# Kernel tuning notes

Hardware: AMD Instinct MI355X
Metric: run time of the kernel (lower is better)

Reference implementation:

```python
import jax, jax.numpy as jnp
import numpy as np

B, S, D_MODEL = 8, 2048, 512
G, V = 2, 320          # num_groups, num_vars
CV_DIM = 256 // G      # proj_dim // num_groups = 128
TAU = 2.0


def setup_inputs() -> dict:
    key = jax.random.key(0)
    k1, k2, k3, k4, k5 = jax.random.split(key, 5)
    hidden_states = jax.random.normal(k1, (B, S, D_MODEL), dtype=jnp.float32)
    # Linear(d_model -> G*V); store as (in, out) for direct matmul
    W = jax.random.normal(k2, (D_MODEL, G * V), dtype=jnp.float32) * (1.0 / np.sqrt(D_MODEL))
    b = jax.random.normal(k3, (G * V,), dtype=jnp.float32) * 0.01
    codevectors = jax.random.normal(k4, (1, G * V, CV_DIM), dtype=jnp.float32)
    # pre-sampled Gumbel(0,1) noise, shape (B*S*G, V)
    u = jax.random.uniform(k5, (B * S * G, V), dtype=jnp.float32,
                           minval=1e-10, maxval=1.0)
    gumbels = -jnp.log(-jnp.log(u))
    return {"hidden_states": hidden_states, "W": W, "b": b,
            "codevectors": codevectors, "gumbels": gumbels}


def reference(hidden_states, W, b, codevectors, gumbels):
    Bs, Ss, _ = hidden_states.shape
    N = Bs * Ss
    # weight projection: (B,S,D) @ (D,G*V) -> (B,S,G*V)
    logits = hidden_states @ W + b
    logits = logits.reshape(N * G, V).astype(jnp.float32)

    # gumbel-softmax, hard=True with straight-through
    y_soft = jax.nn.softmax((logits + gumbels) / TAU, axis=-1)  # (N*G, V)
    idx = jnp.argmax(y_soft, axis=-1)
    y_hard = jax.nn.one_hot(idx, V, dtype=y_soft.dtype)
    codevector_probs = y_hard - jax.lax.stop_gradient(y_soft) + y_soft

    # perplexity from the (noise-free) soft distribution
    soft_dist = jax.nn.softmax(logits.reshape(N, G, V), axis=-1)
    marginal = soft_dist.mean(axis=0)                            # (G, V)
    perplexity = jnp.exp(-jnp.sum(marginal * jnp.log(marginal + 1e-7),
                                  axis=-1)).sum()

    # codebook lookup as weighted sum (equivalent to one-hot gather)
    cv = codevectors.reshape(G, V, CV_DIM)
    probs = codevector_probs.reshape(N, G, V)
    out = jnp.einsum('ngv,gvd->ngd', probs, cv)                  # (N, G, d)
    out = out.reshape(Bs, Ss, G * CV_DIM)
    return out, perplexity
```

## Files before the change

kernel.cpp:

```cpp
#include <hip/hip_runtime.h>

#define M_ROWS 16384
#define K_DIM  512
#define N_COLS 640
#define V_CODES 320
#define CV_DIM 128

typedef _Float16 half8 __attribute__((ext_vector_type(8)));
typedef _Float16 half4v __attribute__((ext_vector_type(4)));
typedef float floatx4 __attribute__((ext_vector_type(4)));

__device__ inline void gll16(const void* g, void* l) {
    __builtin_amdgcn_global_load_lds(
        (const __attribute__((address_space(1))) void*)g,
        (__attribute__((address_space(3))) void*)l, 16, 0, 0);
}

#define SBAR()  __builtin_amdgcn_sched_barrier(0)
#define WAITV(N) asm volatile("s_waitcnt vmcnt(" #N ")" ::: "memory")
#define WAITL() asm volatile("s_waitcnt lgkmcnt(0)" ::: "memory")

__global__ __launch_bounds__(256)
void prepW(const float* __restrict__ W, _Float16* __restrict__ Wt,
           float* __restrict__ marginal) {
    __shared__ float tile[32][33];
    const int b = blockIdx.x, t = threadIdx.x;
    if (b == 320) {
        for (int i = t; i < 640; i += 256) marginal[i] = 0.f;
        return;
    }
    const int n0 = (b % 20) * 32, k0 = (b / 20) * 32;
    {
        const int kk = t >> 3, nn4 = (t & 7) << 2;
        const float4 w = *(const float4*)(W + (size_t)(k0 + kk) * 640 + n0 + nn4);
        tile[kk][nn4 + 0] = w.x; tile[kk][nn4 + 1] = w.y;
        tile[kk][nn4 + 2] = w.z; tile[kk][nn4 + 3] = w.w;
    }
    __syncthreads();
    {
        const int nn = t >> 3, kk4 = (t & 7) << 2;
        half4v h = {(_Float16)tile[kk4 + 0][nn], (_Float16)tile[kk4 + 1][nn],
                    (_Float16)tile[kk4 + 2][nn], (_Float16)tile[kk4 + 3][nn]};
        *(half4v*)(Wt + (size_t)(n0 + nn) * 512 + k0 + kk4) = h;
    }
}

__global__ __launch_bounds__(256, 2)
void fused(const float* __restrict__ A, const _Float16* __restrict__ Bt,
           const float* __restrict__ bias, const float* __restrict__ gum,
           const float* __restrict__ cv, float* __restrict__ out,
           float* __restrict__ marginal) {
    __shared__ _Float16 Bs[2][320 * 32];
    __shared__ _Float16 As[2][64 * 32];
    __shared__ float smarg[320];
    __shared__ float wbest[2][64];
    __shared__ float wsum[2][64];
    __shared__ int   wbidx[2][64];
    __shared__ int   fbidx[64];
    __shared__ float finv[64];

    const int t = threadIdx.x;
    const int wave = t >> 6, lane = t & 63;
    const int bm = blockIdx.x, g = blockIdx.y;
    const int mi = wave >> 1, nh = wave & 1;
    const int c = lane & 15, kq = lane >> 4;

    for (int i = t; i < 320; i += 256) smarg[i] = 0.f;

    floatx4 acc[2][10];
#pragma unroll
    for (int mt = 0; mt < 2; ++mt)
#pragma unroll
        for (int nt = 0; nt < 10; ++nt) acc[mt][nt] = (floatx4){0.f, 0.f, 0.f, 0.f};

    const int am = t >> 2, ad = t & 3;
    const int a_wr = am * 64 + ((ad ^ (am & 3)) << 4);
    const float* Aptr = A + (size_t)(bm * 64 + am) * 512 + ad * 8;

    const _Float16* Bg = Bt + (size_t)g * V_CODES * K_DIM;

    float4 avA0, avA1;
    float4 avN0, avN1;

    auto ISSUE_B = [&](int buf, int k0) {
#pragma unroll
        for (int s = 0; s < 5; ++s) {
            const int q = t + 256 * s;
            const int n = q >> 2, j = q & 3;
            gll16(Bg + (size_t)n * 512 + k0 + ((j ^ (n & 3)) << 3),
                  (char*)(&Bs[buf][0]) + q * 16);
        }
    };
    auto WRITE_A = [&](int buf, const float4& v0, const float4& v1) {
        const half8 h = {(_Float16)v0.x, (_Float16)v0.y, (_Float16)v0.z,
                         (_Float16)v0.w, (_Float16)v1.x, (_Float16)v1.y,
                         (_Float16)v1.z, (_Float16)v1.w};
        *(half8*)((char*)(&As[buf][0]) + a_wr) = h;
    };
    auto COMPUTE = [&](int cur) {
        half8 af[2];
#pragma unroll
        for (int mt = 0; mt < 2; ++mt) {
            const int ra = mi * 32 + mt * 16 + c;
            af[mt] = *(const half8*)((const char*)(&As[cur][0]) +
                      ra * 64 + ((kq ^ (ra & 3)) << 4));
        }
        __builtin_amdgcn_s_setprio(1);
#pragma unroll
        for (int nt = 0; nt < 10; ++nt) {
            const int rb = nh * 160 + nt * 16 + c;
            const half8 bf = *(const half8*)((const char*)(&Bs[cur][0]) +
                              rb * 64 + ((kq ^ (rb & 3)) << 4));
            acc[0][nt] = __builtin_amdgcn_mfma_f32_16x16x32_f16(af[0], bf,
                                                                acc[0][nt], 0, 0, 0);
            acc[1][nt] = __builtin_amdgcn_mfma_f32_16x16x32_f16(af[1], bf,
                                                                acc[1][nt], 0, 0, 0);
        }
        __builtin_amdgcn_s_setprio(0);
    };

    avA0 = *(const float4*)(Aptr + 0);
    avA1 = *(const float4*)(Aptr + 4);
    ISSUE_B(0, 0);
    WRITE_A(0, avA0, avA1);
    avA0 = *(const float4*)(Aptr + 32);
    avA1 = *(const float4*)(Aptr + 36);
    ISSUE_B(1, 32);
    SBAR(); WAITV(7);
    SBAR(); WAITL();
    SBAR(); __builtin_amdgcn_s_barrier(); SBAR();

    for (int kt = 0; kt < 14; ++kt) {
        const int cur = kt & 1;
        COMPUTE(cur);
        SBAR(); __builtin_amdgcn_s_barrier(); SBAR();
        avN0 = *(const float4*)(Aptr + (kt + 2) * 32);
        avN1 = *(const float4*)(Aptr + (kt + 2) * 32 + 4);
        ISSUE_B(cur, (kt + 2) * 32);
        WRITE_A(cur ^ 1, avA0, avA1);
        SBAR(); WAITV(7);
        SBAR(); WAITL();
        SBAR(); __builtin_amdgcn_s_barrier(); SBAR();
        avA0 = avN0; avA1 = avN1;
    }
    COMPUTE(0);
    SBAR(); __builtin_amdgcn_s_barrier(); SBAR();
    WRITE_A(1, avA0, avA1);
    SBAR(); WAITV(0);
    SBAR(); WAITL();
    SBAR(); __builtin_amdgcn_s_barrier(); SBAR();
    COMPUTE(1);

    float bcol[10];
#pragma unroll
    for (int nt = 0; nt < 10; ++nt)
        bcol[nt] = bias[g * V_CODES + nh * 160 + nt * 16 + c];

#pragma unroll
    for (int mt = 0; mt < 2; ++mt) {
#pragma unroll
        for (int rg = 0; rg < 4; ++rg) {
            const int row = mi * 32 + mt * 16 + kq * 4 + rg;
            const float* gr = gum + ((size_t)(bm * 64 + row) * 2 + g) * V_CODES
                              + nh * 160 + c;
            float lg[10];
#pragma unroll
            for (int nt = 0; nt < 10; ++nt) lg[nt] = acc[mt][nt][rg] + bcol[nt];
            float best = -1e30f; int bidx = 0;
#pragma unroll
            for (int nt = 0; nt < 10; ++nt) {
                const float nz = lg[nt] + gr[nt * 16];
                const int v = nh * 160 + nt * 16 + c;
                if (nz > best) { best = nz; bidx = v; }
            }
#pragma unroll
            for (int mask = 1; mask <= 8; mask <<= 1) {
                const float ob = __shfl_xor(best, mask);
                const int   oi = __shfl_xor(bidx, mask);
                if (ob > best || (ob == best && oi < bidx)) { best = ob; bidx = oi; }
            }
            float s = 0.f;
#pragma unroll
            for (int nt = 0; nt < 10; ++nt) {
                const float e = __expf(lg[nt]);
                acc[mt][nt][rg] = e;
                s += e;
            }
#pragma unroll
            for (int mask = 1; mask <= 8; mask <<= 1) s += __shfl_xor(s, mask);
            if (c == 0) {
                wbest[nh][row] = best;
                wbidx[nh][row] = bidx;
                wsum[nh][row]  = s;
            }
        }
    }
    __syncthreads();

    if (t < 64) {
        const float b0 = wbest[0][t]; const int i0 = wbidx[0][t];
        const float b1 = wbest[1][t]; const int i1 = wbidx[1][t];
        fbidx[t] = (b1 > b0 || (b1 == b0 && i1 < i0)) ? i1 : i0;
        finv[t]  = 1.f / (wsum[0][t] + wsum[1][t]);
    }
    __syncthreads();

    float mcon[10];
#pragma unroll
    for (int nt = 0; nt < 10; ++nt) mcon[nt] = 0.f;
#pragma unroll
    for (int mt = 0; mt < 2; ++mt) {
#pragma unroll
        for (int rg = 0; rg < 4; ++rg) {
            const float iv = finv[mi * 32 + mt * 16 + kq * 4 + rg];
#pragma unroll
            for (int nt = 0; nt < 10; ++nt) mcon[nt] += acc[mt][nt][rg] * iv;
        }
    }
#pragma unroll
    for (int nt = 0; nt < 10; ++nt) {
        mcon[nt] += __shfl_xor(mcon[nt], 16);
        mcon[nt] += __shfl_xor(mcon[nt], 32);
    }
    if (lane < 16) {
#pragma unroll
        for (int nt = 0; nt < 10; ++nt)
            atomicAdd(&smarg[nh * 160 + nt * 16 + c], mcon[nt]);
    }
    __syncthreads();
    for (int i = t; i < 320; i += 256)
        atomicAdd(marginal + g * V_CODES + i, smarg[i]);

    if (nh == 0) {
#pragma unroll
        for (int rr = 0; rr < 4; ++rr) {
            const int row = mi * 32 + rr * 8 + (lane >> 3);
            const int bi = fbidx[row];
            const int p = lane & 7;
            const float4* cvp = (const float4*)(cv +
                ((size_t)g * V_CODES + bi) * CV_DIM) + p * 4;
            const float4 v0 = cvp[0], v1 = cvp[1], v2 = cvp[2], v3 = cvp[3];
            float4* op = (float4*)(out + (size_t)(bm * 64 + row) * 256
                                   + g * CV_DIM) + p * 4;
            op[0] = v0; op[1] = v1; op[2] = v2; op[3] = v3;
        }
    }
}

__global__ __launch_bounds__(640)
void finalize(const float* __restrict__ marginal, float* __restrict__ perp_out) {
    __shared__ float terms[640];
    __shared__ float gsum[2];
    const int t = threadIdx.x;

    const float m = marginal[t] * (1.0f / (float)M_ROWS);
    terms[t] = -m * __logf(m + 1e-7f);
    __syncthreads();

    if (t < 128) {
        const int g = t >> 6, lane = t & 63;
        float e = 0.f;
#pragma unroll
        for (int j = 0; j < 5; ++j) e += terms[g * V_CODES + lane + 64 * j];
#pragma unroll
        for (int off = 32; off; off >>= 1) e += __shfl_down(e, off);
        if (lane == 0) gsum[g] = e;
    }
    __syncthreads();
    if (t == 0) perp_out[0] = __expf(gsum[0]) + __expf(gsum[1]);
}

extern "C" void kernel_launch(void* const* d_in, const int* in_sizes, int n_in,
                              void* d_out, int out_size, void* d_ws, size_t ws_size,
                              hipStream_t stream) {
    (void)in_sizes; (void)n_in; (void)out_size; (void)ws_size;
    const float* hs = (const float*)d_in[0];
    const float* W  = (const float*)d_in[1];
    const float* bi = (const float*)d_in[2];
    const float* cv = (const float*)d_in[3];
    const float* gu = (const float*)d_in[4];
    float* out = (float*)d_out;

    _Float16* Wt       = (_Float16*)d_ws;
    float*    marginal = (float*)(Wt + (size_t)N_COLS * K_DIM);

    prepW<<<321, 256, 0, stream>>>(W, Wt, marginal);
    fused<<<dim3(256, 2), 256, 0, stream>>>(hs, Wt, bi, gu, cv, out, marginal);
    finalize<<<1, 640, 0, stream>>>(marginal, out + (size_t)M_ROWS * 256);
}
```

Baseline: 50.49 us.

## Double fused kernel block to 512 threads with one M-tile per wave

Raises the fused GEMM+gumbel kernel from 256 to 512 threads per block with eight waves, so each wave computes one 16-row M tile instead of two. A and B global-to-LDS loads are re-split across the larger block, with a per-wave vmcnt wait because waves issue different numbers of loads. The aim is more waves in flight per CU for latency hiding and fewer accumulator registers per thread. In exchange, each wave does half the MFMA work per LDS A-fragment read, and barrier cost grows with the larger block.

```diff
diff --git a/kernel.cpp b/kernel.cpp
--- a/kernel.cpp
+++ b/kernel.cpp
@@ -45,7 +45,7 @@
     }
 }
 
-__global__ __launch_bounds__(256, 2)
+__global__ __launch_bounds__(512, 4)
 void fused(const float* __restrict__ A, const _Float16* __restrict__ Bt,
            const float* __restrict__ bias, const float* __restrict__ gum,
            const float* __restrict__ cv, float* __restrict__ out,
@@ -65,68 +65,69 @@
     const int mi = wave >> 1, nh = wave & 1;
     const int c = lane & 15, kq = lane >> 4;
 
-    for (int i = t; i < 320; i += 256) smarg[i] = 0.f;
-
-    floatx4 acc[2][10];
-#pragma unroll
-    for (int mt = 0; mt < 2; ++mt)
-#pragma unroll
-        for (int nt = 0; nt < 10; ++nt) acc[mt][nt] = (floatx4){0.f, 0.f, 0.f, 0.f};
-
-    const int am = t >> 2, ad = t & 3;
-    const int a_wr = am * 64 + ((ad ^ (am & 3)) << 4);
-    const float* Aptr = A + (size_t)(bm * 64 + am) * 512 + ad * 8;
+    for (int i = t; i < 320; i += 512) smarg[i] = 0.f;
+
+    floatx4 acc[10];
+#pragma unroll
+    for (int nt = 0; nt < 10; ++nt) acc[nt] = (floatx4){0.f, 0.f, 0.f, 0.f};
+
+    const int am = t >> 3, ad = t & 7;
+    const int a_wr = am * 64 + ((((ad >> 1) ^ (am & 3))) << 4) + (ad & 1) * 8;
+    const float* Aptr = A + (size_t)(bm * 64 + am) * 512 + ad * 4;
 
     const _Float16* Bg = Bt + (size_t)g * V_CODES * K_DIM;
 
-    float4 avA0, avA1;
-    float4 avN0, avN1;
+    float4 avA, avN;
 
     auto ISSUE_B = [&](int buf, int k0) {
-#pragma unroll
-        for (int s = 0; s < 5; ++s) {
-            const int q = t + 256 * s;
+        {
+            const int q = t;
             const int n = q >> 2, j = q & 3;
             gll16(Bg + (size_t)n * 512 + k0 + ((j ^ (n & 3)) << 3),
                   (char*)(&Bs[buf][0]) + q * 16);
         }
-    };
-    auto WRITE_A = [&](int buf, const float4& v0, const float4& v1) {
-        const half8 h = {(_Float16)v0.x, (_Float16)v0.y, (_Float16)v0.z,
-                         (_Float16)v0.w, (_Float16)v1.x, (_Float16)v1.y,
-                         (_Float16)v1.z, (_Float16)v1.w};
-        *(half8*)((char*)(&As[buf][0]) + a_wr) = h;
+        {
+            const int q = t + 512;
+            const int n = q >> 2, j = q & 3;
+            gll16(Bg + (size_t)n * 512 + k0 + ((j ^ (n & 3)) << 3),
+                  (char*)(&Bs[buf][0]) + q * 16);
+        }
+        if (t < 256) {
+            const int q = t + 1024;
+            const int n = q >> 2, j = q & 3;
+            gll16(Bg + (size_t)n * 512 + k0 + ((j ^ (n & 3)) << 3),
+                  (char*)(&Bs[buf][0]) + q * 16);
+        }
+    };
+    auto WRITE_A = [&](int buf, const float4& v) {
+        const half4v h = {(_Float16)v.x, (_Float16)v.y, (_Float16)v.z,
+                          (_Float16)v.w};
+        *(half4v*)((char*)(&As[buf][0]) + a_wr) = h;
     };
     auto COMPUTE = [&](int cur) {
-        half8 af[2];
-#pragma unroll
-        for (int mt = 0; mt < 2; ++mt) {
-            const int ra = mi * 32 + mt * 16 + c;
-            af[mt] = *(const half8*)((const char*)(&As[cur][0]) +
-                      ra * 64 + ((kq ^ (ra & 3)) << 4));
-        }
+        const int ra = mi * 16 + c;
+        const half8 af = *(const half8*)((const char*)(&As[cur][0]) +
+                          ra * 64 + ((kq ^ (ra & 3)) << 4));
         __builtin_amdgcn_s_setprio(1);
 #pragma unroll
         for (int nt = 0; nt < 10; ++nt) {
             const int rb = nh * 160 + nt * 16 + c;
             const half8 bf = *(const half8*)((const char*)(&Bs[cur][0]) +
                               rb * 64 + ((kq ^ (rb & 3)) << 4));
-            acc[0][nt] = __builtin_amdgcn_mfma_f32_16x16x32_f16(af[0], bf,
-                                                                acc[0][nt], 0, 0, 0);
-            acc[1][nt] = __builtin_amdgcn_mfma_f32_16x16x32_f16(af[1], bf,
-                                                                acc[1][nt], 0, 0, 0);
+            acc[nt] = __builtin_amdgcn_mfma_f32_16x16x32_f16(af, bf, acc[nt], 0, 0, 0);
         }
         __builtin_amdgcn_s_setprio(0);
     };
-
-    avA0 = *(const float4*)(Aptr + 0);
-    avA1 = *(const float4*)(Aptr + 4);
+    auto WAITPW = [&]() {
+        if (wave < 4) { WAITV(4); } else { WAITV(3); }
+    };
+
+    avA = *(const float4*)(Aptr + 0);
     ISSUE_B(0, 0);
-    WRITE_A(0, avA0, avA1);
-    avA0 = *(const float4*)(Aptr + 32);
-    avA1 = *(const float4*)(Aptr + 36);
+    WRITE_A(0, avA);
     ISSUE_B(1, 32);
-    SBAR(); WAITV(7);
+    avA = *(const float4*)(Aptr + 32);
+    SBAR(); WAITPW();
     SBAR(); WAITL();
     SBAR(); __builtin_amdgcn_s_barrier(); SBAR();
 
@@ -134,18 +135,17 @@
         const int cur = kt & 1;
         COMPUTE(cur);
         SBAR(); __builtin_amdgcn_s_barrier(); SBAR();
-        avN0 = *(const float4*)(Aptr + (kt + 2) * 32);
-        avN1 = *(const float4*)(Aptr + (kt + 2) * 32 + 4);
         ISSUE_B(cur, (kt + 2) * 32);
-        WRITE_A(cur ^ 1, avA0, avA1);
-        SBAR(); WAITV(7);
+        avN = *(const float4*)(Aptr + (kt + 2) * 32);
+        WRITE_A(cur ^ 1, avA);
+        SBAR(); WAITPW();
         SBAR(); WAITL();
         SBAR(); __builtin_amdgcn_s_barrier(); SBAR();
-        avA0 = avN0; avA1 = avN1;
+        avA = avN;
     }
     COMPUTE(0);
     SBAR(); __builtin_amdgcn_s_barrier(); SBAR();
-    WRITE_A(1, avA0, avA1);
+    WRITE_A(1, avA);
     SBAR(); WAITV(0);
     SBAR(); WAITL();
     SBAR(); __builtin_amdgcn_s_barrier(); SBAR();
@@ -157,42 +157,39 @@
         bcol[nt] = bias[g * V_CODES + nh * 160 + nt * 16 + c];
 
 #pragma unroll
-    for (int mt = 0; mt < 2; ++mt) {
-#pragma unroll
-        for (int rg = 0; rg < 4; ++rg) {
-            const int row = mi * 32 + mt * 16 + kq * 4 + rg;
-            const float* gr = gum + ((size_t)(bm * 64 + row) * 2 + g) * V_CODES
-                              + nh * 160 + c;
-            float lg[10];
-#pragma unroll
-            for (int nt = 0; nt < 10; ++nt) lg[nt] = acc[mt][nt][rg] + bcol[nt];
-            float best = -1e30f; int bidx = 0;
-#pragma unroll
-            for (int nt = 0; nt < 10; ++nt) {
-                const float nz = lg[nt] + gr[nt * 16];
-                const int v = nh * 160 + nt * 16 + c;
-                if (nz > best) { best = nz; bidx = v; }
-            }
-#pragma unroll
-            for (int mask = 1; mask <= 8; mask <<= 1) {
-                const float ob = __shfl_xor(best, mask);
-                const int   oi = __shfl_xor(bidx, mask);
-                if (ob > best || (ob == best && oi < bidx)) { best = ob; bidx = oi; }
-            }
-            float s = 0.f;
-#pragma unroll
-            for (int nt = 0; nt < 10; ++nt) {
-                const float e = __expf(lg[nt]);
-                acc[mt][nt][rg] = e;
-                s += e;
-            }
-#pragma unroll
-            for (int mask = 1; mask <= 8; mask <<= 1) s += __shfl_xor(s, mask);
-            if (c == 0) {
-                wbest[nh][row] = best;
-                wbidx[nh][row] = bidx;
-                wsum[nh][row]  = s;
-            }
+    for (int rg = 0; rg < 4; ++rg) {
+        const int row = mi * 16 + kq * 4 + rg;
+        const float* gr = gum + ((size_t)(bm * 64 + row) * 2 + g) * V_CODES
+                          + nh * 160 + c;
+        float lg[10];
+#pragma unroll
+        for (int nt = 0; nt < 10; ++nt) lg[nt] = acc[nt][rg] + bcol[nt];
+        float best = -1e30f; int bidx = 0;
+#pragma unroll
+        for (int nt = 0; nt < 10; ++nt) {
+            const float nz = lg[nt] + gr[nt * 16];
+            const int v = nh * 160 + nt * 16 + c;
+            if (nz > best) { best = nz; bidx = v; }
+        }
+#pragma unroll
+        for (int mask = 1; mask <= 8; mask <<= 1) {
+            const float ob = __shfl_xor(best, mask);
+            const int   oi = __shfl_xor(bidx, mask);
+            if (ob > best || (ob == best && oi < bidx)) { best = ob; bidx = oi; }
+        }
+        float s = 0.f;
+#pragma unroll
+        for (int nt = 0; nt < 10; ++nt) {
+            const float e = __expf(lg[nt]);
+            acc[nt][rg] = e;
+            s += e;
+        }
+#pragma unroll
+        for (int mask = 1; mask <= 8; mask <<= 1) s += __shfl_xor(s, mask);
+        if (c == 0) {
+            wbest[nh][row] = best;
+            wbidx[nh][row] = bidx;
+            wsum[nh][row]  = s;
         }
     }
     __syncthreads();
@@ -209,13 +206,10 @@
 #pragma unroll
     for (int nt = 0; nt < 10; ++nt) mcon[nt] = 0.f;
 #pragma unroll
-    for (int mt = 0; mt < 2; ++mt) {
-#pragma unroll
-        for (int rg = 0; rg < 4; ++rg) {
-            const float iv = finv[mi * 32 + mt * 16 + kq * 4 + rg];
-#pragma unroll
-            for (int nt = 0; nt < 10; ++nt) mcon[nt] += acc[mt][nt][rg] * iv;
-        }
+    for (int rg = 0; rg < 4; ++rg) {
+        const float iv = finv[mi * 16 + kq * 4 + rg];
+#pragma unroll
+        for (int nt = 0; nt < 10; ++nt) mcon[nt] += acc[nt][rg] * iv;
     }
 #pragma unroll
     for (int nt = 0; nt < 10; ++nt) {
@@ -228,13 +222,13 @@
             atomicAdd(&smarg[nh * 160 + nt * 16 + c], mcon[nt]);
     }
     __syncthreads();
-    for (int i = t; i < 320; i += 256)
+    for (int i = t; i < 320; i += 512)
         atomicAdd(marginal + g * V_CODES + i, smarg[i]);
 
     if (nh == 0) {
 #pragma unroll
-        for (int rr = 0; rr < 4; ++rr) {
-            const int row = mi * 32 + rr * 8 + (lane >> 3);
+        for (int rr = 0; rr < 2; ++rr) {
+            const int row = mi * 16 + rr * 8 + (lane >> 3);
             const int bi = fbidx[row];
             const int p = lane & 7;
             const float4* cvp = (const float4*)(cv +
@@ -285,6 +279,6 @@
     float*    marginal = (float*)(Wt + (size_t)N_COLS * K_DIM);
 
     prepW<<<321, 256, 0, stream>>>(W, Wt, marginal);
-    fused<<<dim3(256, 2), 256, 0, stream>>>(hs, Wt, bi, gu, cv, out, marginal);
+    fused<<<dim3(256, 2), 512, 0, stream>>>(hs, Wt, bi, gu, cv, out, marginal);
     finalize<<<1, 640, 0, stream>>>(marginal, out + (size_t)M_ROWS * 256);
 }
```

Measured after the change: 50.87 us. About the same (+0.7%).
